# Performance work log

Measured on AMD Instinct MI355X. Metric: run time of the kernel, lower is better.

The kernel has to match this reference:

```python
import jax, jax.numpy as jnp
import numpy as np

N_LAYER = 4
N_EMBD = 768
N_HEAD = 12
B, T = 4, 1024  # T = 4 * t, t = 256 (block_size)
EPS = 1e-5


def layernorm(x, g, b):
    mu = jnp.mean(x, axis=-1, keepdims=True)
    var = jnp.var(x, axis=-1, keepdims=True)
    return (x - mu) * jax.lax.rsqrt(var + EPS) * g + b


def setup_inputs() -> dict:
    key = jax.random.key(0)
    ks = jax.random.split(key, 20)
    C, L, H = N_EMBD, N_LAYER, 4 * N_EMBD
    std = 0.02
    inp = {
        "x": jax.random.normal(ks[0], (B, T, C), dtype=jnp.float32),
        "ln1_g": jnp.ones((L, C), jnp.float32),
        "ln1_b": jnp.zeros((L, C), jnp.float32),
        "Wq": std * jax.random.normal(ks[1], (L, C, C), jnp.float32),
        "bq": jnp.zeros((L, C), jnp.float32),
        "Wk": std * jax.random.normal(ks[2], (L, C, C), jnp.float32),
        "bk": jnp.zeros((L, C), jnp.float32),
        "Wv": std * jax.random.normal(ks[3], (L, C, C), jnp.float32),
        "bv": jnp.zeros((L, C), jnp.float32),
        "Wp": std * jax.random.normal(ks[4], (L, C, C), jnp.float32),
        "bp": jnp.zeros((L, C), jnp.float32),
        "ln2_g": jnp.ones((L, C), jnp.float32),
        "ln2_b": jnp.zeros((L, C), jnp.float32),
        "W1": std * jax.random.normal(ks[5], (L, C, H), jnp.float32),
        "b1": jnp.zeros((L, H), jnp.float32),
        "W2": std * jax.random.normal(ks[6], (L, H, C), jnp.float32),
        "b2": jnp.zeros((L, C), jnp.float32),
    }
    return inp


def _forward(x, ln1_g, ln1_b, Wq, bq, Wk, bk, Wv, bv, Wp, bp, ln2_g, ln2_b, W1, b1, W2, b2):
    Bx, Tx, C = x.shape
    hd = C // N_HEAD
    t = Tx // 4
    # cross-conditional mask: causal tril(t,t) tiled 4x4 over the 4 streams
    mask = jnp.tile(jnp.tril(jnp.ones((t, t), dtype=bool)), (4, 4))  # [T, T]
    scale = 1.0 / np.sqrt(hd).astype(np.float32)

    def block(h, p):
        (g1, b1g, wq, bqv, wk, bkv, wv, bvv, wp, bpv, g2, b2g, w1, b1v, w2, b2v) = p
        a_in = layernorm(h, g1, b1g)
        q = (a_in @ wq + bqv).reshape(Bx, Tx, N_HEAD, hd).transpose(0, 2, 1, 3)
        k = (a_in @ wk + bkv).reshape(Bx, Tx, N_HEAD, hd).transpose(0, 2, 1, 3)
        v = (a_in @ wv + bvv).reshape(Bx, Tx, N_HEAD, hd).transpose(0, 2, 1, 3)
        att = jnp.einsum('bhqd,bhkd->bhqk', q, k) * scale
        att = jnp.where(mask, att, -jnp.inf)
        att = jax.nn.softmax(att, axis=-1)
        y = jnp.einsum('bhqk,bhkd->bhqd', att, v)
        y = y.transpose(0, 2, 1, 3).reshape(Bx, Tx, C)
        h = h + (y @ wp + bpv)
        m_in = layernorm(h, g2, b2g)
        m = jax.nn.gelu(m_in @ w1 + b1v, approximate=False) @ w2 + b2v
        return h + m, None

    params = (ln1_g, ln1_b, Wq, bq, Wk, bk, Wv, bv, Wp, bp, ln2_g, ln2_b, W1, b1, W2, b2)
    x, _ = jax.lax.scan(block, x, params)
    return x


def reference(x, ln1_g, ln1_b, Wq, bq, Wk, bk, Wv, bv, Wp, bp, ln2_g, ln2_b, W1, b1, W2, b2):
    return _forward(x, ln1_g, ln1_b, Wq, bq, Wk, bk, Wv, bv, Wp, bp, ln2_g, ln2_b, W1, b1, W2, b2)
```

## Files before the change

### kernel.cpp

```cpp
#include <hip/hip_runtime.h>
#include <hip/hip_bf16.h>
#include <math.h>

typedef __hip_bfloat16 bf16;
typedef __attribute__((ext_vector_type(8))) short bf16x8;
typedef __attribute__((ext_vector_type(4))) short s16x4;
typedef __attribute__((ext_vector_type(4))) unsigned short u16x4;
typedef __attribute__((ext_vector_type(8))) unsigned short u16x8;
typedef __attribute__((ext_vector_type(4))) float f32x4;

#define CDIM 768
#define HDIM 64
#define NHEAD 12
#define TSEQ 1024
#define MROWS 4096
#define HID 3072
#define QKVN 2304

__device__ inline void gld16(const void* g, void* l) {
  __builtin_amdgcn_global_load_lds((const __attribute__((address_space(1))) void*)g,
                                   (__attribute__((address_space(3))) void*)l, 16, 0, 0);
}
__device__ inline short f2bs(float f) { bf16 h = __float2bfloat16(f); return *reinterpret_cast<short*>(&h); }

__global__ __launch_bounds__(256) void k_trans(const float* __restrict__ Wq, const float* __restrict__ Wk,
                        const float* __restrict__ Wv, const float* __restrict__ Wp,
                        const float* __restrict__ W1, const float* __restrict__ W2,
                        const float* __restrict__ bq, const float* __restrict__ bk,
                        const float* __restrict__ bv,
                        bf16* __restrict__ wqkv, bf16* __restrict__ wtp,
                        bf16* __restrict__ wt1, bf16* __restrict__ wt2,
                        float* __restrict__ bqkv) {
  __shared__ float t[64][65];
  int blk = blockIdx.x;
  int l = blk / 1737; blk -= l * 1737;
  Wq += (size_t)l * CDIM * CDIM; Wk += (size_t)l * CDIM * CDIM;
  Wv += (size_t)l * CDIM * CDIM; Wp += (size_t)l * CDIM * CDIM;
  W1 += (size_t)l * CDIM * HID;  W2 += (size_t)l * HID * CDIM;
  bq += (size_t)l * CDIM; bk += (size_t)l * CDIM; bv += (size_t)l * CDIM;
  wqkv += (size_t)l * QKVN * CDIM; wtp += (size_t)l * CDIM * CDIM;
  wt1  += (size_t)l * CDIM * HID;  wt2 += (size_t)l * CDIM * HID;
  bqkv += (size_t)l * QKVN;
  int tid = threadIdx.x;
  if (blk >= 1728) {
    int i = (blk - 1728) * 256 + tid;
    if (i < QKVN) bqkv[i] = (i < CDIM) ? bq[i] : (i < 2 * CDIM) ? bk[i - CDIM] : bv[i - 2 * CDIM];
    return;
  }
  const float* src; bf16* dst; int K, N, n0, k0;
  if (blk < 432) {
    int w = blk / 144, id = blk % 144;
    src = (w == 0) ? Wq : (w == 1) ? Wk : Wv;
    dst = wqkv + (size_t)w * CDIM * CDIM;
    K = CDIM; N = CDIM;
    n0 = (id % 12) * 64; k0 = (id / 12) * 64;
  } else if (blk < 576) {
    int id = blk - 432;
    src = Wp; dst = wtp; K = CDIM; N = CDIM;
    n0 = (id % 12) * 64; k0 = (id / 12) * 64;
  } else if (blk < 1152) {
    int id = blk - 576;
    src = W1; dst = wt1; K = CDIM; N = HID;
    n0 = (id % 48) * 64; k0 = (id / 48) * 64;
  } else {
    int id = blk - 1152;
    src = W2; dst = wt2; K = HID; N = CDIM;
    n0 = (id % 12) * 64; k0 = (id / 12) * 64;
  }
  int c = tid & 63, r0 = tid >> 6;
  const float* sp = src + (size_t)(k0 + r0) * N + n0 + c;
  #pragma unroll
  for (int i = 0; i < 16; i++)
    t[r0 + 4 * i][c] = sp[(size_t)(4 * i) * N];
  __syncthreads();
  int n = tid >> 2, kk = (tid & 3) * 16;
  bf16* dp = dst + (size_t)(n0 + n) * K + k0 + kk;
  #pragma unroll
  for (int s2 = 0; s2 < 2; s2++) {
    u16x8 o;
    #pragma unroll
    for (int j = 0; j < 8; j++)
      o[j] = (unsigned short)f2bs(t[kk + 8 * s2 + j][n]);
    *(u16x8*)(dp + 8 * s2) = o;
  }
}

__global__ __launch_bounds__(256) void k_ln(const float* __restrict__ h, const float* __restrict__ g,
                                            const float* __restrict__ b, bf16* __restrict__ out) {
  int wave = threadIdx.x >> 6, lane = threadIdx.x & 63;
  int row = blockIdx.x * 4 + wave;
  const float4* hr = (const float4*)(h + (size_t)row * CDIM);
  float4 v[3];
  float s = 0.f, ss = 0.f;
  #pragma unroll
  for (int i = 0; i < 3; i++) {
    v[i] = hr[lane * 3 + i];
    s  += v[i].x + v[i].y + v[i].z + v[i].w;
    ss += v[i].x * v[i].x + v[i].y * v[i].y + v[i].z * v[i].z + v[i].w * v[i].w;
  }
  #pragma unroll
  for (int off = 32; off > 0; off >>= 1) {
    s  += __shfl_xor(s, off, 64);
    ss += __shfl_xor(ss, off, 64);
  }
  float mu = s * (1.0f / CDIM);
  float var = ss * (1.0f / CDIM) - mu * mu;
  float rstd = rsqrtf(var + 1e-5f);
  const float4* gp = (const float4*)g;
  const float4* bp = (const float4*)b;
  s16x4* orow = (s16x4*)(out + (size_t)row * CDIM);
  #pragma unroll
  for (int i = 0; i < 3; i++) {
    float4 gg = gp[lane * 3 + i], bb = bp[lane * 3 + i];
    s16x4 o;
    o.x = f2bs((v[i].x - mu) * rstd * gg.x + bb.x);
    o.y = f2bs((v[i].y - mu) * rstd * gg.y + bb.y);
    o.z = f2bs((v[i].z - mu) * rstd * gg.z + bb.z);
    o.w = f2bs((v[i].w - mu) * rstd * gg.w + bb.w);
    orow[lane * 3 + i] = o;
  }
}


template <int BM, int BN, int EPI>
__global__ __launch_bounds__(256) void k_gemmT(const bf16* __restrict__ A, const bf16* __restrict__ Bt,
                                               const float* __restrict__ bias,
                                               void* __restrict__ outv, bf16* __restrict__ out2,
                                               int M, int N, int K) {
  constexpr int MR = BM / 32, NR = BN / 32;
  __shared__ __align__(16) bf16 As[BM * 64];
  __shared__ __align__(16) bf16 Bs[BN * 64];
  int tid = threadIdx.x;
  int m0 = blockIdx.x * BM, n0 = blockIdx.y * BN;
  int wave = tid >> 6, lane = tid & 63;
  int wr = wave >> 1, wc = wave & 1;
  int lrow = lane & 15, quad = lane >> 4;
  int sw = lrow & 7;
  f32x4 zz = {0.f, 0.f, 0.f, 0.f};
  f32x4 acc[MR][NR];
  #pragma unroll
  for (int i = 0; i < MR; i++)
    #pragma unroll
    for (int j = 0; j < NR; j++) acc[i][j] = zz;
  const bf16* Ag = A + (size_t)m0 * K;
  const bf16* Bg = Bt + (size_t)n0 * K;
  for (int k0 = 0; k0 < K; k0 += 64) {
    __syncthreads();
    #pragma unroll
    for (int i = 0; i < BM / 32; i++) {
      int idx = i * 256 + tid;
      int row = idx >> 3, c = idx & 7;
      gld16(Ag + (size_t)row * K + k0 + ((c ^ (row & 7)) * 8), As + idx * 8);
    }
    #pragma unroll
    for (int i = 0; i < BN / 32; i++) {
      int idx = i * 256 + tid;
      int row = idx >> 3, c = idx & 7;
      gld16(Bg + (size_t)row * K + k0 + ((c ^ (row & 7)) * 8), Bs + idx * 8);
    }
    __syncthreads();
    #pragma unroll
    for (int kc = 0; kc < 2; kc++) {
      int g = kc * 4 + quad;
      bf16x8 af[MR], bfr[NR];
      #pragma unroll
      for (int mi = 0; mi < MR; mi++)
        af[mi] = *(const bf16x8*)(As + (wr * (BM / 2) + mi * 16 + lrow) * 64 + ((g ^ sw) * 8));
      #pragma unroll
      for (int ni = 0; ni < NR; ni++)
        bfr[ni] = *(const bf16x8*)(Bs + (wc * (BN / 2) + ni * 16 + lrow) * 64 + ((g ^ sw) * 8));
      #pragma unroll
      for (int mi = 0; mi < MR; mi++)
        #pragma unroll
        for (int ni = 0; ni < NR; ni++)
          acc[mi][ni] = __builtin_amdgcn_mfma_f32_16x16x32_bf16(af[mi], bfr[ni], acc[mi][ni], 0, 0, 0);
    }
  }
  #pragma unroll
  for (int ni = 0; ni < NR; ni++) {
    int gc = n0 + wc * (BN / 2) + ni * 16 + lrow;
    float bval = bias[gc];
    #pragma unroll
    for (int mi = 0; mi < MR; mi++) {
      if (EPI == 3 && gc >= 1536) {
        int dcol = gc - 1536, h2 = dcol >> 6, dd = dcol & 63;
        int grow0 = m0 + wr * (BM / 2) + mi * 16 + quad * 4;
        u16x4 o;
        o.x = (unsigned short)f2bs(acc[mi][ni][0] + bval);
        o.y = (unsigned short)f2bs(acc[mi][ni][1] + bval);
        o.z = (unsigned short)f2bs(acc[mi][ni][2] + bval);
        o.w = (unsigned short)f2bs(acc[mi][ni][3] + bval);
        int bh2 = (grow0 >> 10) * NHEAD + h2;
        *(u16x4*)(out2 + ((size_t)bh2 * HDIM + dd) * TSEQ + (grow0 & 1023)) = o;
      } else {
        #pragma unroll
        for (int r = 0; r < 4; r++) {
          int grow = m0 + wr * (BM / 2) + mi * 16 + quad * 4 + r;
          float vv = acc[mi][ni][r] + bval;
          if (EPI == 1) {
            float u = 1.5957691216f * (vv + 0.044715f * vv * vv * vv);
            vv = vv / (1.0f + __expf(-u));
          }
          if (EPI == 2) {
            float* hp = (float*)outv + (size_t)grow * N + gc;
            *hp = *hp + vv;
          } else {
            ((bf16*)outv)[(size_t)grow * N + gc] = __float2bfloat16(vv);
          }
        }
      }
    }
  }
}

__global__ __launch_bounds__(256) void k_attn(const bf16* __restrict__ qkv, const bf16* __restrict__ vt,
                                              bf16* __restrict__ y) {
  int bh = blockIdx.x;
  int b = bh / NHEAD, hh = bh % NHEAD;
  int qc = blockIdx.y ^ 3;
  int tid = threadIdx.x;
  int wave = tid >> 6, lane = tid & 63;
  int lrow = lane & 15, quad = lane >> 4;
  int sw = lrow & 7;
  int q0 = qc * 64 + wave * 16;
  int qmod = q0 & 255;
  int qcmod = (qc * 64) & 255;

  const size_t rstride = QKVN;
  const bf16* qbase = qkv + (size_t)(b * TSEQ) * rstride + hh * HDIM;
  const bf16* kbase = qbase + CDIM;
  const bf16* vtb = vt + (size_t)bh * HDIM * TSEQ;

  bf16x8 qf[2];
  #pragma unroll
  for (int kc = 0; kc < 2; kc++)
    qf[kc] = *(const bf16x8*)(qbase + (size_t)(q0 + lrow) * rstride + kc * 32 + quad * 8);

  f32x4 zz = {0.f, 0.f, 0.f, 0.f};
  f32x4 Oacc[4];
  #pragma unroll
  for (int j = 0; j < 4; j++) Oacc[j] = zz;
  float m = -1e30f, l = 0.f;

  __shared__ __align__(16) bf16 Ks[64 * 64];
  __shared__ __align__(16) bf16 Vs[64 * 64];
  __shared__ __align__(16) bf16 Pl[4][16 * 64];

  for (int kt = 0; kt < 16; kt++) {
    int k0 = kt * 64;
    int kmod = k0 & 255;
    if (kmod > qcmod + 63) continue;
    __syncthreads();
    #pragma unroll
    for (int i = 0; i < 2; i++) {
      int idx = i * 256 + tid;
      int row = idx >> 3, c = idx & 7;
      gld16(kbase + (size_t)(k0 + row) * rstride + ((c ^ (row & 7)) * 8), Ks + idx * 8);
      gld16(vtb + (size_t)row * TSEQ + k0 + ((c ^ (row & 7)) * 8), Vs + idx * 8);
    }
    __syncthreads();
    if (kmod > qmod + 15) continue;

    f32x4 s[4];
    #pragma unroll
    for (int sub = 0; sub < 4; sub++) {
      s[sub] = zz;
      #pragma unroll
      for (int kc = 0; kc < 2; kc++) {
        int g = kc * 4 + quad;
        bf16x8 kf = *(const bf16x8*)(Ks + (sub * 16 + lrow) * 64 + ((g ^ sw) * 8));
        s[sub] = __builtin_amdgcn_mfma_f32_16x16x32_bf16(kf, qf[kc], s[sub], 0, 0, 0);
      }
    }
    bool partial = (kmod + 63 > qmod);
    int qrel = qmod + lrow;
    #pragma unroll
    for (int sub = 0; sub < 4; sub++)
      #pragma unroll
      for (int r = 0; r < 4; r++) {
        float sv = s[sub][r] * 0.125f;
        if (partial && (kmod + sub * 16 + quad * 4 + r > qrel)) sv = -1e30f;
        s[sub][r] = sv;
      }
    float mx = fmaxf(fmaxf(fmaxf(s[0][0], s[0][1]), fmaxf(s[0][2], s[0][3])),
                     fmaxf(fmaxf(s[1][0], s[1][1]), fmaxf(s[1][2], s[1][3])));
    mx = fmaxf(mx, fmaxf(fmaxf(fmaxf(s[2][0], s[2][1]), fmaxf(s[2][2], s[2][3])),
                         fmaxf(fmaxf(s[3][0], s[3][1]), fmaxf(s[3][2], s[3][3]))));
    mx = fmaxf(mx, __shfl_xor(mx, 16, 64));
    mx = fmaxf(mx, __shfl_xor(mx, 32, 64));
    float mnew = fmaxf(m, mx);
    float alpha = __expf(m - mnew);
    m = mnew;
    float p[4][4];
    float rs = 0.f;
    #pragma unroll
    for (int sub = 0; sub < 4; sub++)
      #pragma unroll
      for (int r = 0; r < 4; r++) {
        p[sub][r] = __expf(s[sub][r] - mnew);
        rs += p[sub][r];
      }
    rs += __shfl_xor(rs, 16, 64);
    rs += __shfl_xor(rs, 32, 64);
    l = l * alpha + rs;
    #pragma unroll
    for (int r = 0; r < 4; r++) {
      float ar = __shfl(alpha, quad * 4 + r, 16);
      #pragma unroll
      for (int j = 0; j < 4; j++) Oacc[j][r] *= ar;
    }
    bf16* Pw = (bf16*)Pl[wave];
    #pragma unroll
    for (int sub = 0; sub < 4; sub++) {
      u16x4 o;
      o.x = (unsigned short)f2bs(p[sub][0]);
      o.y = (unsigned short)f2bs(p[sub][1]);
      o.z = (unsigned short)f2bs(p[sub][2]);
      o.w = (unsigned short)f2bs(p[sub][3]);
      int ch = sub * 2 + (quad >> 1);
      *(u16x4*)(Pw + lrow * 64 + ((ch ^ sw) * 8) + 4 * (quad & 1)) = o;
    }
    bf16x8 pf[2];
    #pragma unroll
    for (int kc = 0; kc < 2; kc++) {
      int g = kc * 4 + quad;
      pf[kc] = *(const bf16x8*)(Pw + lrow * 64 + ((g ^ sw) * 8));
    }
    #pragma unroll
    for (int j = 0; j < 4; j++)
      #pragma unroll
      for (int kc = 0; kc < 2; kc++) {
        int g = kc * 4 + quad;
        bf16x8 vf = *(const bf16x8*)(Vs + (j * 16 + lrow) * 64 + ((g ^ sw) * 8));
        Oacc[j] = __builtin_amdgcn_mfma_f32_16x16x32_bf16(pf[kc], vf, Oacc[j], 0, 0, 0);
      }
  }
  #pragma unroll
  for (int r = 0; r < 4; r++) {
    float linv = 1.0f / __shfl(l, quad * 4 + r, 16);
    bf16* yp = y + (size_t)(b * TSEQ + q0 + quad * 4 + r) * CDIM + hh * HDIM;
    #pragma unroll
    for (int j = 0; j < 4; j++)
      yp[j * 16 + lrow] = __float2bfloat16(Oacc[j][r] * linv);
  }
}

extern "C" void kernel_launch(void* const* d_in, const int* in_sizes, int n_in,
                              void* d_out, int out_size, void* d_ws, size_t ws_size,
                              hipStream_t stream) {
  const float* x    = (const float*)d_in[0];
  const float* ln1g = (const float*)d_in[1];
  const float* ln1b = (const float*)d_in[2];
  const float* Wq   = (const float*)d_in[3];
  const float* bq   = (const float*)d_in[4];
  const float* Wk   = (const float*)d_in[5];
  const float* bk   = (const float*)d_in[6];
  const float* Wv   = (const float*)d_in[7];
  const float* bv   = (const float*)d_in[8];
  const float* Wp   = (const float*)d_in[9];
  const float* bp   = (const float*)d_in[10];
  const float* ln2g = (const float*)d_in[11];
  const float* ln2b = (const float*)d_in[12];
  const float* W1   = (const float*)d_in[13];
  const float* b1   = (const float*)d_in[14];
  const float* W2   = (const float*)d_in[15];
  const float* b2   = (const float*)d_in[16];

  char* ws = (char*)d_ws;
  size_t off = 0;
  float* h    = (float*)(ws + off); off += (size_t)MROWS * CDIM * 4;
  bf16* a     = (bf16*)(ws + off);  off += (size_t)MROWS * CDIM * 2;
  bf16* qkvb  = (bf16*)(ws + off);  off += (size_t)MROWS * QKVN * 2;
  bf16* yb    = (bf16*)(ws + off);  off += (size_t)MROWS * CDIM * 2;
  bf16* vt    = (bf16*)(ws + off);  off += (size_t)4 * NHEAD * HDIM * TSEQ * 2;
  bf16* m1    = qkvb;

  const size_t szQkv = (size_t)QKVN * CDIM * 2;
  const size_t szP   = (size_t)CDIM * CDIM * 2;
  const size_t szW1  = (size_t)CDIM * HID * 2;
  const size_t szW2  = (size_t)CDIM * HID * 2;
  const size_t szB   = (size_t)QKVN * 4;
  const size_t wlayer = szQkv + szP + szW1 + szW2 + szB;
  bool hoist = ws_size >= off + 4 * wlayer + 4096;
  int nW = hoist ? 4 : 1;

  bf16* wqkv  = (bf16*)(ws + off);  off += nW * szQkv;
  bf16* wtp   = (bf16*)(ws + off);  off += nW * szP;
  bf16* wt1   = (bf16*)(ws + off);  off += nW * szW1;
  bf16* wt2   = (bf16*)(ws + off);  off += nW * szW2;
  float* bqkv = (float*)(ws + off); off += nW * szB;

  int n = MROWS * CDIM;
  hipMemcpyAsync(h, x, (size_t)n * sizeof(float), hipMemcpyDeviceToDevice, stream);

  if (hoist)
    k_trans<<<dim3(4 * 1737), dim3(256), 0, stream>>>(Wq, Wk, Wv, Wp, W1, W2, bq, bk, bv,
                                                      wqkv, wtp, wt1, wt2, bqkv);

  for (int l = 0; l < 4; l++) {
    int wl = hoist ? l : 0;
    if (!hoist)
      k_trans<<<dim3(1737), dim3(256), 0, stream>>>(
          Wq + (size_t)l * CDIM * CDIM, Wk + (size_t)l * CDIM * CDIM,
          Wv + (size_t)l * CDIM * CDIM, Wp + (size_t)l * CDIM * CDIM,
          W1 + (size_t)l * CDIM * HID, W2 + (size_t)l * HID * CDIM,
          bq + (size_t)l * CDIM, bk + (size_t)l * CDIM, bv + (size_t)l * CDIM,
          wqkv, wtp, wt1, wt2, bqkv);
    const bf16* wqkvl = wqkv + (size_t)wl * QKVN * CDIM;
    const bf16* wtpl  = wtp  + (size_t)wl * CDIM * CDIM;
    const bf16* wt1l  = wt1  + (size_t)wl * CDIM * HID;
    const bf16* wt2l  = wt2  + (size_t)wl * CDIM * HID;
    const float* bqkvl = bqkv + (size_t)wl * QKVN;

    k_ln<<<dim3(MROWS / 4), dim3(256), 0, stream>>>(h, ln1g + l * CDIM, ln1b + l * CDIM, a);

    k_gemmT<64, 128, 3><<<dim3(MROWS / 64, QKVN / 128), dim3(256), 0, stream>>>(
        a, wqkvl, bqkvl, qkvb, vt, MROWS, QKVN, CDIM);

    k_attn<<<dim3(4 * NHEAD, 16), dim3(256), 0, stream>>>(qkvb, vt, yb);

    k_gemmT<64, 64, 2><<<dim3(MROWS / 64, CDIM / 64), dim3(256), 0, stream>>>(
        yb, wtpl, bp + (size_t)l * CDIM, h, nullptr, MROWS, CDIM, CDIM);

    k_ln<<<dim3(MROWS / 4), dim3(256), 0, stream>>>(h, ln2g + l * CDIM, ln2b + l * CDIM, a);

    k_gemmT<64, 128, 1><<<dim3(MROWS / 64, HID / 128), dim3(256), 0, stream>>>(
        a, wt1l, b1 + (size_t)l * HID, m1, nullptr, MROWS, HID, CDIM);

    k_gemmT<64, 64, 2><<<dim3(MROWS / 64, CDIM / 64), dim3(256), 0, stream>>>(
        m1, wt2l, b2 + (size_t)l * CDIM, h, nullptr, MROWS, CDIM, HID);
  }

  hipMemcpyAsync(d_out, h, (size_t)n * sizeof(float), hipMemcpyDeviceToDevice, stream);
}
```

Baseline: 758.6 us.

## Double-buffer K/V tiles in attention with prefetch and skip-aware iteration

The attention kernel now double-buffers K and V tiles in shared memory and issues the async global-to-LDS loads for the next needed tile before computing on the current one, using explicit vmcnt waits and raw barriers. Tile iteration jumps directly over masked-out key tiles instead of looping and continuing. MFMA sections are wrapped with s_setprio so matrix work gets issue priority. This doubles K/V LDS usage, which may reduce occupancy, and relies on hand-placed waitcnt counts being correct.

```diff
diff --git a/kernel.cpp b/kernel.cpp
--- a/kernel.cpp
+++ b/kernel.cpp
@@ -22,6 +22,13 @@
                                    (__attribute__((address_space(3))) void*)l, 16, 0, 0);
 }
 __device__ inline short f2bs(float f) { bf16 h = __float2bfloat16(f); return *reinterpret_cast<short*>(&h); }
+__device__ inline void vw4() { asm volatile("s_waitcnt vmcnt(4)" ::: "memory"); }
+__device__ inline void vw0() { asm volatile("s_waitcnt vmcnt(0)" ::: "memory"); }
+__device__ inline void BAR() {
+  asm volatile("" ::: "memory");
+  __builtin_amdgcn_s_barrier();
+  asm volatile("" ::: "memory");
+}
 
 __global__ __launch_bounds__(256) void k_trans(const float* __restrict__ Wq, const float* __restrict__ Wk,
                         const float* __restrict__ Wv, const float* __restrict__ Wp,
@@ -224,7 +231,7 @@
   int sw = lrow & 7;
   int q0 = qc * 64 + wave * 16;
   int qmod = q0 & 255;
-  int qcmod = (qc * 64) & 255;
+  int qsel = qc & 3;
 
   const size_t rstride = QKVN;
   const bf16* qbase = qkv + (size_t)(b * TSEQ) * rstride + hh * HDIM;
@@ -242,99 +249,116 @@
   for (int j = 0; j < 4; j++) Oacc[j] = zz;
   float m = -1e30f, l = 0.f;
 
-  __shared__ __align__(16) bf16 Ks[64 * 64];
-  __shared__ __align__(16) bf16 Vs[64 * 64];
+  __shared__ __align__(16) bf16 Ks[2][64 * 64];
+  __shared__ __align__(16) bf16 Vs[2][64 * 64];
   __shared__ __align__(16) bf16 Pl[4][16 * 64];
 
-  for (int kt = 0; kt < 16; kt++) {
-    int k0 = kt * 64;
-    int kmod = k0 & 255;
-    if (kmod > qcmod + 63) continue;
-    __syncthreads();
-    #pragma unroll
-    for (int i = 0; i < 2; i++) {
-      int idx = i * 256 + tid;
-      int row = idx >> 3, c = idx & 7;
-      gld16(kbase + (size_t)(k0 + row) * rstride + ((c ^ (row & 7)) * 8), Ks + idx * 8);
-      gld16(vtb + (size_t)row * TSEQ + k0 + ((c ^ (row & 7)) * 8), Vs + idx * 8);
-    }
-    __syncthreads();
-    if (kmod > qmod + 15) continue;
-
-    f32x4 s[4];
-    #pragma unroll
-    for (int sub = 0; sub < 4; sub++) {
-      s[sub] = zz;
+#define STAGEKV(kt_, bi)                                                                     \
+  {                                                                                          \
+    int k0_ = (kt_) * 64;                                                                    \
+    _Pragma("unroll")                                                                        \
+    for (int i = 0; i < 2; i++) {                                                            \
+      int idx = i * 256 + tid;                                                               \
+      int row = idx >> 3, c = idx & 7;                                                       \
+      gld16(kbase + (size_t)(k0_ + row) * rstride + ((c ^ (row & 7)) * 8), Ks[bi] + idx * 8);\
+      gld16(vtb + (size_t)row * TSEQ + k0_ + ((c ^ (row & 7)) * 8), Vs[bi] + idx * 8);       \
+    }                                                                                        \
+  }
+
+  STAGEKV(0, 0);
+  int cur = 0;
+  int kt = 0;
+  while (kt >= 0) {
+    int nkt = ((kt & 3) == qsel) ? ((kt & ~3) + 4) : kt + 1;
+    bool have_next = (nkt < 16);
+    if (have_next) { STAGEKV(nkt, cur ^ 1); vw4(); } else { vw0(); }
+    BAR();
+    int kmod = (kt * 64) & 255;
+    if (!(kmod > qmod + 15)) {
+      f32x4 s[4];
+      __builtin_amdgcn_s_setprio(1);
+      #pragma unroll
+      for (int sub = 0; sub < 4; sub++) {
+        s[sub] = zz;
+        #pragma unroll
+        for (int kc = 0; kc < 2; kc++) {
+          int g = kc * 4 + quad;
+          bf16x8 kf = *(const bf16x8*)(Ks[cur] + (sub * 16 + lrow) * 64 + ((g ^ sw) * 8));
+          s[sub] = __builtin_amdgcn_mfma_f32_16x16x32_bf16(kf, qf[kc], s[sub], 0, 0, 0);
+        }
+      }
+      __builtin_amdgcn_s_setprio(0);
+      bool partial = (kmod + 63 > qmod);
+      int qrel = qmod + lrow;
+      #pragma unroll
+      for (int sub = 0; sub < 4; sub++)
+        #pragma unroll
+        for (int r = 0; r < 4; r++) {
+          float sv = s[sub][r] * 0.125f;
+          if (partial && (kmod + sub * 16 + quad * 4 + r > qrel)) sv = -1e30f;
+          s[sub][r] = sv;
+        }
+      float mx = fmaxf(fmaxf(fmaxf(s[0][0], s[0][1]), fmaxf(s[0][2], s[0][3])),
+                       fmaxf(fmaxf(s[1][0], s[1][1]), fmaxf(s[1][2], s[1][3])));
+      mx = fmaxf(mx, fmaxf(fmaxf(fmaxf(s[2][0], s[2][1]), fmaxf(s[2][2], s[2][3])),
+                           fmaxf(fmaxf(s[3][0], s[3][1]), fmaxf(s[3][2], s[3][3]))));
+      mx = fmaxf(mx, __shfl_xor(mx, 16, 64));
+      mx = fmaxf(mx, __shfl_xor(mx, 32, 64));
+      float mnew = fmaxf(m, mx);
+      float alpha = __expf(m - mnew);
+      m = mnew;
+      float p[4][4];
+      float rs = 0.f;
+      #pragma unroll
+      for (int sub = 0; sub < 4; sub++)
+        #pragma unroll
+        for (int r = 0; r < 4; r++) {
+          p[sub][r] = __expf(s[sub][r] - mnew);
+          rs += p[sub][r];
+        }
+      rs += __shfl_xor(rs, 16, 64);
+      rs += __shfl_xor(rs, 32, 64);
+      l = l * alpha + rs;
+      #pragma unroll
+      for (int r = 0; r < 4; r++) {
+        float ar = __shfl(alpha, quad * 4 + r, 16);
+        #pragma unroll
+        for (int j = 0; j < 4; j++) Oacc[j][r] *= ar;
+      }
+      bf16* Pw = (bf16*)Pl[wave];
+      #pragma unroll
+      for (int sub = 0; sub < 4; sub++) {
+        u16x4 o;
+        o.x = (unsigned short)f2bs(p[sub][0]);
+        o.y = (unsigned short)f2bs(p[sub][1]);
+        o.z = (unsigned short)f2bs(p[sub][2]);
+        o.w = (unsigned short)f2bs(p[sub][3]);
+        int ch = sub * 2 + (quad >> 1);
+        *(u16x4*)(Pw + lrow * 64 + ((ch ^ sw) * 8) + 4 * (quad & 1)) = o;
+      }
+      bf16x8 pf[2];
       #pragma unroll
       for (int kc = 0; kc < 2; kc++) {
         int g = kc * 4 + quad;
-        bf16x8 kf = *(const bf16x8*)(Ks + (sub * 16 + lrow) * 64 + ((g ^ sw) * 8));
-        s[sub] = __builtin_amdgcn_mfma_f32_16x16x32_bf16(kf, qf[kc], s[sub], 0, 0, 0);
+        pf[kc] = *(const bf16x8*)(Pw + lrow * 64 + ((g ^ sw) * 8));
       }
+      __builtin_amdgcn_s_setprio(1);
+      #pragma unroll
+      for (int j = 0; j < 4; j++)
+        #pragma unroll
+        for (int kc = 0; kc < 2; kc++) {
+          int g = kc * 4 + quad;
+          bf16x8 vf = *(const bf16x8*)(Vs[cur] + (j * 16 + lrow) * 64 + ((g ^ sw) * 8));
+          Oacc[j] = __builtin_amdgcn_mfma_f32_16x16x32_bf16(pf[kc], vf, Oacc[j], 0, 0, 0);
+        }
+      __builtin_amdgcn_s_setprio(0);
     }
-    bool partial = (kmod + 63 > qmod);
-    int qrel = qmod + lrow;
-    #pragma unroll
-    for (int sub = 0; sub < 4; sub++)
-      #pragma unroll
-      for (int r = 0; r < 4; r++) {
-        float sv = s[sub][r] * 0.125f;
-        if (partial && (kmod + sub * 16 + quad * 4 + r > qrel)) sv = -1e30f;
-        s[sub][r] = sv;
-      }
-    float mx = fmaxf(fmaxf(fmaxf(s[0][0], s[0][1]), fmaxf(s[0][2], s[0][3])),
-                     fmaxf(fmaxf(s[1][0], s[1][1]), fmaxf(s[1][2], s[1][3])));
-    mx = fmaxf(mx, fmaxf(fmaxf(fmaxf(s[2][0], s[2][1]), fmaxf(s[2][2], s[2][3])),
-                         fmaxf(fmaxf(s[3][0], s[3][1]), fmaxf(s[3][2], s[3][3]))));
-    mx = fmaxf(mx, __shfl_xor(mx, 16, 64));
-    mx = fmaxf(mx, __shfl_xor(mx, 32, 64));
-    float mnew = fmaxf(m, mx);
-    float alpha = __expf(m - mnew);
-    m = mnew;
-    float p[4][4];
-    float rs = 0.f;
-    #pragma unroll
-    for (int sub = 0; sub < 4; sub++)
-      #pragma unroll
-      for (int r = 0; r < 4; r++) {
-        p[sub][r] = __expf(s[sub][r] - mnew);
-        rs += p[sub][r];
-      }
-    rs += __shfl_xor(rs, 16, 64);
-    rs += __shfl_xor(rs, 32, 64);
-    l = l * alpha + rs;
-    #pragma unroll
-    for (int r = 0; r < 4; r++) {
-      float ar = __shfl(alpha, quad * 4 + r, 16);
-      #pragma unroll
-      for (int j = 0; j < 4; j++) Oacc[j][r] *= ar;
-    }
-    bf16* Pw = (bf16*)Pl[wave];
-    #pragma unroll
-    for (int sub = 0; sub < 4; sub++) {
-      u16x4 o;
-      o.x = (unsigned short)f2bs(p[sub][0]);
-      o.y = (unsigned short)f2bs(p[sub][1]);
-      o.z = (unsigned short)f2bs(p[sub][2]);
-      o.w = (unsigned short)f2bs(p[sub][3]);
-      int ch = sub * 2 + (quad >> 1);
-      *(u16x4*)(Pw + lrow * 64 + ((ch ^ sw) * 8) + 4 * (quad & 1)) = o;
-    }
-    bf16x8 pf[2];
-    #pragma unroll
-    for (int kc = 0; kc < 2; kc++) {
-      int g = kc * 4 + quad;
-      pf[kc] = *(const bf16x8*)(Pw + lrow * 64 + ((g ^ sw) * 8));
-    }
-    #pragma unroll
-    for (int j = 0; j < 4; j++)
-      #pragma unroll
-      for (int kc = 0; kc < 2; kc++) {
-        int g = kc * 4 + quad;
-        bf16x8 vf = *(const bf16x8*)(Vs + (j * 16 + lrow) * 64 + ((g ^ sw) * 8));
-        Oacc[j] = __builtin_amdgcn_mfma_f32_16x16x32_bf16(pf[kc], vf, Oacc[j], 0, 0, 0);
-      }
-  }
+    BAR();
+    cur ^= 1;
+    kt = have_next ? nkt : -1;
+  }
+#undef STAGEKV
+
   #pragma unroll
   for (int r = 0; r < 4; r++) {
     float linv = 1.0f / __shfl(l, quad * 4 + r, 16);
```

New measurement: 785.3 us. +3.5%, slower.
